# Performance work log

Measured on AMD Instinct MI355X. Metric: run time of the kernel, lower is better.

The kernel has to match this reference:

```python
import jax, jax.numpy as jnp
import numpy as np

DIM = 1024
NUM_HEADS = 16
HEAD_DIM = DIM // NUM_HEADS
ROPE_BASE = 10000.0


def _rope_tables(seq_len, head_dim, dtype):
    # inv_freq over even indices, then freqs duplicated (cat(freqs, freqs))
    inv_freq = 1.0 / (ROPE_BASE ** (jnp.arange(0, head_dim, 2, dtype=jnp.float32) / head_dim))
    t = jnp.arange(seq_len, dtype=jnp.float32)
    freqs = jnp.einsum('i,j->ij', t, inv_freq)          # [N, head_dim/2]
    emb = jnp.concatenate([freqs, freqs], axis=-1)      # [N, head_dim]
    return jnp.cos(emb).astype(dtype), jnp.sin(emb).astype(dtype)


def _rotate_half(x):
    x1, x2 = jnp.split(x, 2, axis=-1)
    return jnp.concatenate([-x2, x1], axis=-1)


def setup_inputs() -> dict:
    key = jax.random.key(0)
    k1, k2, k3 = jax.random.split(key, 3)
    B, N = 2, 2048
    x = jax.random.normal(k1, (B, N, DIM), dtype=jnp.float32)
    w_qkv = jax.random.normal(k2, (3 * DIM, DIM), dtype=jnp.float32) * (DIM ** -0.5)
    w_out = jax.random.normal(k3, (DIM, DIM), dtype=jnp.float32) * (DIM ** -0.5)
    return {"x": x, "w_qkv": w_qkv, "w_out": w_out}


def reference(x, w_qkv, w_out):
    B, N, C = x.shape
    scale = HEAD_DIM ** -0.5
    qkv = x @ w_qkv.T                                   # [B, N, 3*C]
    qkv = qkv.reshape(B, N, 3, NUM_HEADS, HEAD_DIM)
    qkv = jnp.transpose(qkv, (2, 0, 3, 1, 4))           # [3, B, H, N, hd]
    q, k, v = qkv[0], qkv[1], qkv[2]

    cos, sin = _rope_tables(N, HEAD_DIM, x.dtype)       # [N, hd] each
    q = q * cos + _rotate_half(q) * sin
    k = k * cos + _rotate_half(k) * sin

    attn = jnp.einsum('bhqd,bhkd->bhqk', q, k) * scale  # [B, H, N, N]
    attn = jax.nn.softmax(attn, axis=-1)
    out = jnp.einsum('bhqk,bhkd->bhqd', attn, v)        # [B, H, N, hd]
    out = jnp.transpose(out, (0, 2, 1, 3)).reshape(B, N, C)
    return out @ w_out.T
```

## Files before the change

### kernel.cpp

```cpp
#include <hip/hip_runtime.h>
#include <stdint.h>


#define BATCH 2
#define SEQ   2048
#define DIM_C 1024
#define NHEAD 16
#define HD    64
#define MTOT  (BATCH * SEQ)
#define NQKV  (3 * DIM_C)
#define QSCALE 0.1803368801111204f

typedef _Float16 h8 __attribute__((ext_vector_type(8)));
typedef _Float16 h4v __attribute__((ext_vector_type(4)));
typedef float    f4 __attribute__((ext_vector_type(4)));

#if __has_builtin(__builtin_amdgcn_exp2f)
#define EXP2(x) __builtin_amdgcn_exp2f(x)
#else
#define EXP2(x) exp2f(x)
#endif

__device__ __forceinline__ f4 mfma16(h8 a, h8 b, f4 c) {
  return __builtin_amdgcn_mfma_f32_16x16x32_f16(a, b, c, 0, 0, 0);
}

__device__ __forceinline__ void gload16(const _Float16* g, _Float16* l) {
  __builtin_amdgcn_global_load_lds(
      (const __attribute__((address_space(1))) void*)g,
      (__attribute__((address_space(3))) void*)l, 16, 0, 0);
}

__global__ void cvt_kernel(const float* __restrict__ src, _Float16* __restrict__ dst, int n4) {
  int stride = gridDim.x * blockDim.x;
  for (int i = blockIdx.x * blockDim.x + threadIdx.x; i < n4; i += stride) {
    float4 v = reinterpret_cast<const float4*>(src)[i];
    h4v o = {(_Float16)v.x, (_Float16)v.y, (_Float16)v.z, (_Float16)v.w};
    reinterpret_cast<h4v*>(dst)[i] = o;
  }
}

__global__ void rope_table_kernel(float* __restrict__ cosT, float* __restrict__ sinT) {
  int idx = blockIdx.x * blockDim.x + threadIdx.x;
  int n = idx >> 5, j = idx & 31;
  float inv = powf(10000.0f, -(float)(2 * j) / 64.0f);
  float a = (float)n * inv;
  cosT[idx] = cosf(a);
  sinT[idx] = sinf(a);
}

template <int OUT_F16>
__global__ __launch_bounds__(256) void gemm_nt(const _Float16* __restrict__ A,
                                               const _Float16* __restrict__ Bm,
                                               void* __restrict__ Cv,
                                               int M, int N, int K) {
  __shared__ _Float16 Ah[2][128 * 32];
  __shared__ _Float16 Bh[2][128 * 32];
  const int tid = threadIdx.x;
  const int wave = tid >> 6, lane = tid & 63;
  const int lr = lane & 15, lg = lane >> 4;
  const int m0 = blockIdx.y * 128, n0 = blockIdx.x * 128;
  const int wr = (wave >> 1) * 64, wc = (wave & 1) * 64;

  const f4 zf = {0.f, 0.f, 0.f, 0.f};
  f4 acc[4][4];
#pragma unroll
  for (int i = 0; i < 4; ++i)
#pragma unroll
    for (int j = 0; j < 4; ++j) acc[i][j] = zf;

  const _Float16* Ab = A + (size_t)m0 * K;
  const _Float16* Bb = Bm + (size_t)n0 * K;

  auto stage = [&](int ks, int bi) {
#pragma unroll
    for (int it = 0; it < 2; ++it) {
      int c = tid + it * 256;
      int row = c >> 2, part = c & 3;
      gload16(Ab + (size_t)row * K + ks * 32 + part * 8, &Ah[bi][c * 8]);
      gload16(Bb + (size_t)row * K + ks * 32 + part * 8, &Bh[bi][c * 8]);
    }
  };

  stage(0, 0);
  const int ksteps = K >> 5;
  for (int ks = 0; ks < ksteps; ++ks) {
    __syncthreads();
    int cur = ks & 1;
    if (ks + 1 < ksteps) stage(ks + 1, cur ^ 1);

    h8 af[4], bf[4];
#pragma unroll
    for (int i = 0; i < 4; ++i) af[i] = *(const h8*)&Ah[cur][(wr + i * 16 + lr) * 32 + lg * 8];
#pragma unroll
    for (int j = 0; j < 4; ++j) bf[j] = *(const h8*)&Bh[cur][(wc + j * 16 + lr) * 32 + lg * 8];
#pragma unroll
    for (int i = 0; i < 4; ++i)
#pragma unroll
      for (int j = 0; j < 4; ++j) acc[i][j] = mfma16(af[i], bf[j], acc[i][j]);
  }

#pragma unroll
  for (int i = 0; i < 4; ++i)
#pragma unroll
    for (int j = 0; j < 4; ++j)
#pragma unroll
      for (int r = 0; r < 4; ++r) {
        size_t row = (size_t)(m0 + wr + i * 16 + lg * 4 + r);
        int col = n0 + wc + j * 16 + lr;
        if (OUT_F16)
          ((_Float16*)Cv)[row * N + col] = (_Float16)acc[i][j][r];
        else
          ((float*)Cv)[row * N + col] = acc[i][j][r];
      }
}

__global__ void rope_apply_kernel(const _Float16* __restrict__ qkv,
                                  const float* __restrict__ cosT,
                                  const float* __restrict__ sinT,
                                  _Float16* __restrict__ qh,
                                  _Float16* __restrict__ kh,
                                  _Float16* __restrict__ vh) {
  int idx = blockIdx.x * blockDim.x + threadIdx.x;
  int c8 = idx & 3;
  int t = idx >> 2;
  int h = t & 15;
  t >>= 4;
  int s = t % 3;
  int m = t / 3;
  int b = m >> 11, n = m & 2047;

  const _Float16* src = qkv + (size_t)m * NQKV + s * DIM_C + h * HD + c8 * 8;
  h8 x1 = *(const h8*)src;
  h8 x2 = *(const h8*)(src + 32);
  size_t o = ((size_t)((b * NHEAD + h) * SEQ + n)) * HD + c8 * 8;

  if (s == 2) {
    *(h8*)(vh + o) = x1;
    *(h8*)(vh + o + 32) = x2;
  } else {
    f4 cs0 = *(const f4*)(cosT + n * 32 + c8 * 8);
    f4 cs1 = *(const f4*)(cosT + n * 32 + c8 * 8 + 4);
    f4 sn0 = *(const f4*)(sinT + n * 32 + c8 * 8);
    f4 sn1 = *(const f4*)(sinT + n * 32 + c8 * 8 + 4);
    float scl = (s == 0) ? QSCALE : 1.0f;
    _Float16* dst = (s == 0) ? qh : kh;
    h8 o1, o2;
#pragma unroll
    for (int j = 0; j < 8; ++j) {
      float cv = (j < 4) ? cs0[j] : cs1[j - 4];
      float sv = (j < 4) ? sn0[j] : sn1[j - 4];
      float a1 = (float)x1[j], a2 = (float)x2[j];
      o1[j] = (_Float16)((a1 * cv - a2 * sv) * scl);
      o2[j] = (_Float16)((a2 * cv + a1 * sv) * scl);
    }
    *(h8*)(dst + o) = o1;
    *(h8*)(dst + o + 32) = o2;
  }
}

__global__ void vtrans_kernel(const _Float16* __restrict__ v, _Float16* __restrict__ vt) {
  int blk = blockIdx.x;
  int bh = blk >> 6, nt = blk & 63;
  int d = threadIdx.x & 63, w = threadIdx.x >> 6;
  int n0 = nt * 32 + w * 8;
  const _Float16* src = v + (size_t)bh * SEQ * HD;
  _Float16* dst = vt + ((size_t)bh * HD + d) * SEQ;
  h8 o;
#pragma unroll
  for (int j = 0; j < 8; ++j) o[j] = src[(size_t)(n0 + j) * HD + d];
  *(h8*)(dst + n0) = o;
}

__global__ __launch_bounds__(256) void attn_kernel(const _Float16* __restrict__ qh,
                                                   const _Float16* __restrict__ kh,
                                                   const _Float16* __restrict__ vt,
                                                   _Float16* __restrict__ aoh) {
  __shared__ _Float16 Kt[2][64 * 64];
  __shared__ _Float16 Vt[2][64 * 64];
  __shared__ _Float16 PlA[4][32][40], PlB[4][32][40];

  const int tid = threadIdx.x, wave = tid >> 6, lane = tid & 63;
  const int lr = lane & 15, lg = lane >> 4;
  const int bh = blockIdx.x >> 4;
  const int qt = blockIdx.x & 15;
  const int b = bh >> 4, h = bh & 15;

  const _Float16* Qb = qh + (size_t)bh * SEQ * HD;
  const _Float16* Kb = kh + (size_t)bh * SEQ * HD;
  const _Float16* Vb = vt + (size_t)bh * HD * SEQ;
  const int q0 = qt * 128 + wave * 32;

  const int cOf0 = ((lg) ^ (lr & 7)) * 8;
  const int cOf1 = ((4 + lg) ^ (lr & 7)) * 8;

  h8 aq[2][2];
#pragma unroll
  for (int r2 = 0; r2 < 2; ++r2)
#pragma unroll
    for (int c = 0; c < 2; ++c)
      aq[r2][c] = *(const h8*)(Qb + (size_t)(q0 + r2 * 16 + lr) * HD + c * 32 + lg * 8);

  float m_s[2] = {-1e30f, -1e30f}, l_s[2] = {0.f, 0.f};
  const f4 zf = {0.f, 0.f, 0.f, 0.f};
  f4 acc[2][4];
#pragma unroll
  for (int r2 = 0; r2 < 2; ++r2)
#pragma unroll
    for (int dt = 0; dt < 4; ++dt) acc[r2][dt] = zf;

  auto stage = [&](int kt, int bi) {
    const _Float16* Ks = Kb + (size_t)kt * 64 * HD;
    const _Float16* Vs = Vb + kt * 64;
#pragma unroll
    for (int it = 0; it < 2; ++it) {
      int c = tid + it * 256;
      int row = c >> 3, part = c & 7;
      int sp = part ^ (row & 7);
      gload16(Ks + (size_t)row * HD + sp * 8, &Kt[bi][c * 8]);
      gload16(Vs + (size_t)row * SEQ + sp * 8, &Vt[bi][c * 8]);
    }
  };

  stage(0, 0);
  for (int kt = 0; kt < SEQ / 64; ++kt) {
    __syncthreads();
    const int cur = kt & 1;
    if (kt + 1 < SEQ / 64) stage(kt + 1, cur ^ 1);

    const _Float16* Kbuf = &Kt[cur][0];
    const _Float16* Vbuf = &Vt[cur][0];
    h8 bk[4][2], vb[4][2];
#pragma unroll
    for (int ct = 0; ct < 4; ++ct) {
      bk[ct][0] = *(const h8*)(Kbuf + (ct * 16 + lr) * 64 + cOf0);
      bk[ct][1] = *(const h8*)(Kbuf + (ct * 16 + lr) * 64 + cOf1);
    }
#pragma unroll
    for (int dt = 0; dt < 4; ++dt) {
      vb[dt][0] = *(const h8*)(Vbuf + (dt * 16 + lr) * 64 + cOf0);
      vb[dt][1] = *(const h8*)(Vbuf + (dt * 16 + lr) * 64 + cOf1);
    }

#pragma unroll
    for (int r2 = 0; r2 < 2; ++r2) {
      f4 St[4];
      __builtin_amdgcn_s_setprio(1);
#pragma unroll
      for (int ct = 0; ct < 4; ++ct) {
        f4 z = mfma16(bk[ct][0], aq[r2][0], zf);
        St[ct] = mfma16(bk[ct][1], aq[r2][1], z);
      }
      __builtin_amdgcn_s_setprio(0);
      float pmax = fmaxf(fmaxf(fmaxf(St[0][0], St[0][1]), fmaxf(St[0][2], St[0][3])),
                         fmaxf(fmaxf(St[1][0], St[1][1]), fmaxf(St[1][2], St[1][3])));
      float pmax2 = fmaxf(fmaxf(fmaxf(St[2][0], St[2][1]), fmaxf(St[2][2], St[2][3])),
                          fmaxf(fmaxf(St[3][0], St[3][1]), fmaxf(St[3][2], St[3][3])));
      pmax = fmaxf(pmax, pmax2);
      pmax = fmaxf(pmax, __shfl_xor(pmax, 16));
      pmax = fmaxf(pmax, __shfl_xor(pmax, 32));

      bool grow = pmax > m_s[r2] + 8.f;
      if (__ballot(grow)) {
        float mn = fmaxf(m_s[r2], pmax);
        float al = EXP2(m_s[r2] - mn);
        m_s[r2] = mn;
        l_s[r2] *= al;
#pragma unroll
        for (int dt = 0; dt < 4; ++dt)
#pragma unroll
          for (int r = 0; r < 4; ++r) acc[r2][dt][r] *= al;
      }

      float rsum = 0.f;
#pragma unroll
      for (int ct = 0; ct < 4; ++ct)
#pragma unroll
        for (int r = 0; r < 4; ++r) {
          float p = EXP2(St[ct][r] - m_s[r2]);
          St[ct][r] = p;
          rsum += p;
        }
      rsum += __shfl_xor(rsum, 16);
      rsum += __shfl_xor(rsum, 32);
      l_s[r2] += rsum;

#pragma unroll
      for (int ct = 0; ct < 4; ++ct) {
        h4v pk = {(_Float16)St[ct][0], (_Float16)St[ct][1],
                  (_Float16)St[ct][2], (_Float16)St[ct][3]};
        if (ct < 2)
          *(h4v*)&PlA[wave][r2 * 16 + lr][ct * 16 + lg * 4] = pk;
        else
          *(h4v*)&PlB[wave][r2 * 16 + lr][(ct - 2) * 16 + lg * 4] = pk;
      }
    }

    __builtin_amdgcn_s_setprio(1);
#pragma unroll
    for (int r2 = 0; r2 < 2; ++r2)
#pragma unroll
      for (int c = 0; c < 2; ++c) {
        h8 pa = (c == 0) ? *(const h8*)&PlA[wave][r2 * 16 + lr][lg * 8]
                         : *(const h8*)&PlB[wave][r2 * 16 + lr][lg * 8];
#pragma unroll
        for (int dt = 0; dt < 4; ++dt)
          acc[r2][dt] = mfma16(vb[dt][c], pa, acc[r2][dt]);
      }
    __builtin_amdgcn_s_setprio(0);
  }

#pragma unroll
  for (int r2 = 0; r2 < 2; ++r2) {
    float inv = 1.0f / l_s[r2];
    int q = q0 + r2 * 16 + lr;
#pragma unroll
    for (int dt = 0; dt < 4; ++dt) {
      h4v o = {(_Float16)(acc[r2][dt][0] * inv), (_Float16)(acc[r2][dt][1] * inv),
               (_Float16)(acc[r2][dt][2] * inv), (_Float16)(acc[r2][dt][3] * inv)};
      *(h4v*)&aoh[((size_t)(b * SEQ + q)) * DIM_C + h * HD + dt * 16 + lg * 4] = o;
    }
  }
}

extern "C" void kernel_launch(void* const* d_in, const int* in_sizes, int n_in,
                              void* d_out, int out_size, void* d_ws, size_t ws_size,
                              hipStream_t stream) {
  const float* x     = (const float*)d_in[0];
  const float* w_qkv = (const float*)d_in[1];
  const float* w_out = (const float*)d_in[2];
  float* out = (float*)d_out;

  char* w = (char*)d_ws;
  _Float16* xh    = (_Float16*)(w + 0);
  _Float16* wqkvh = (_Float16*)(w + 8388608);
  _Float16* wouth = (_Float16*)(w + 14680064);
  _Float16* qkvh  = (_Float16*)(w + 16777216);
  _Float16* qhp   = (_Float16*)(w + 41943040);
  _Float16* khp   = (_Float16*)(w + 50331648);
  _Float16* vhp   = (_Float16*)(w + 58720256);
  _Float16* aohp  = (_Float16*)(w + 67108864);
  float*    cosT  = (float*)(w + 75497472);
  float*    sinT  = (float*)(w + 75759616);
  _Float16* vtp   = (_Float16*)(w + 16777216);

  cvt_kernel<<<1024, 256, 0, stream>>>(x, xh, MTOT * DIM_C / 4);
  cvt_kernel<<<1024, 256, 0, stream>>>(w_qkv, wqkvh, NQKV * DIM_C / 4);
  cvt_kernel<<<512, 256, 0, stream>>>(w_out, wouth, DIM_C * DIM_C / 4);
  rope_table_kernel<<<SEQ * 32 / 256, 256, 0, stream>>>(cosT, sinT);

  gemm_nt<1><<<dim3(NQKV / 128, MTOT / 128), 256, 0, stream>>>(
      xh, wqkvh, (void*)qkvh, MTOT, NQKV, DIM_C);

  rope_apply_kernel<<<MTOT * 3 * NHEAD * 4 / 256, 256, 0, stream>>>(
      qkvh, cosT, sinT, qhp, khp, vhp);

  vtrans_kernel<<<32 * 64, 256, 0, stream>>>(vhp, vtp);

  attn_kernel<<<32 * (SEQ / 128), 256, 0, stream>>>(qhp, khp, vtp, aohp);

  gemm_nt<0><<<dim3(DIM_C / 128, MTOT / 128), 256, 0, stream>>>(
      aohp, wouth, (void*)out, MTOT, DIM_C, DIM_C);
}
```

Before: 156.7 us.

## Split attention KV range across two blocks and pass P through registers

The attention kernel now splits each query tile's 2048 keys into two halves handled by separate blocks. This doubles the grid from 512 to 1024 blocks to improve occupancy on the GPU's compute units, and each half writes partial outputs plus its row max and sum. A new merge kernel combines the two halves with softmax rescaling. The P matrix is also now moved into the MFMA operand layout with packed conversions and cross-lane shuffles instead of a round trip through shared memory. This removes LDS traffic, at the cost of an extra kernel launch and extra global memory traffic for the partials.

Measured after the change: 217.8 us. +39.0%, slower.

```diff
diff --git a/kernel.cpp b/kernel.cpp
--- a/kernel.cpp
+++ b/kernel.cpp
@@ -14,6 +14,7 @@
 typedef _Float16 h8 __attribute__((ext_vector_type(8)));
 typedef _Float16 h4v __attribute__((ext_vector_type(4)));
 typedef float    f4 __attribute__((ext_vector_type(4)));
+typedef unsigned int u4v __attribute__((ext_vector_type(4)));
 
 #if __has_builtin(__builtin_amdgcn_exp2f)
 #define EXP2(x) __builtin_amdgcn_exp2f(x)
@@ -23,6 +24,13 @@
 
 __device__ __forceinline__ f4 mfma16(h8 a, h8 b, f4 c) {
   return __builtin_amdgcn_mfma_f32_16x16x32_f16(a, b, c, 0, 0, 0);
+}
+
+__device__ __forceinline__ unsigned pk2(float a, float b) {
+  auto t = __builtin_amdgcn_cvt_pkrtz(a, b);
+  unsigned u;
+  __builtin_memcpy(&u, &t, 4);
+  return u;
 }
 
 __device__ __forceinline__ void gload16(const _Float16* g, _Float16* l) {
@@ -172,17 +180,20 @@
   *(h8*)(dst + n0) = o;
 }
 
-__global__ __launch_bounds__(256) void attn_kernel(const _Float16* __restrict__ qh,
-                                                   const _Float16* __restrict__ kh,
-                                                   const _Float16* __restrict__ vt,
-                                                   _Float16* __restrict__ aoh) {
+__global__ __launch_bounds__(256, 4) void attn_kernel(const _Float16* __restrict__ qh,
+                                                      const _Float16* __restrict__ kh,
+                                                      const _Float16* __restrict__ vt,
+                                                      _Float16* __restrict__ Opart,
+                                                      float* __restrict__ ml) {
   __shared__ _Float16 Kt[2][64 * 64];
   __shared__ _Float16 Vt[2][64 * 64];
-  __shared__ _Float16 PlA[4][32][40], PlB[4][32][40];
 
   const int tid = threadIdx.x, wave = tid >> 6, lane = tid & 63;
   const int lr = lane & 15, lg = lane >> 4;
-  const int bh = blockIdx.x >> 4;
+  const bool hi32 = (lane & 32) != 0;
+  const bool o16 = (lane & 16) != 0;
+  const int bh = blockIdx.x >> 5;
+  const int half = (blockIdx.x >> 4) & 1;
   const int qt = blockIdx.x & 15;
   const int b = bh >> 4, h = bh & 15;
 
@@ -190,6 +201,7 @@
   const _Float16* Kb = kh + (size_t)bh * SEQ * HD;
   const _Float16* Vb = vt + (size_t)bh * HD * SEQ;
   const int q0 = qt * 128 + wave * 32;
+  const int t0 = half * 16;
 
   const int cOf0 = ((lg) ^ (lr & 7)) * 8;
   const int cOf1 = ((4 + lg) ^ (lr & 7)) * 8;
@@ -222,11 +234,11 @@
     }
   };
 
-  stage(0, 0);
-  for (int kt = 0; kt < SEQ / 64; ++kt) {
+  stage(t0, 0);
+  for (int t = 0; t < 16; ++t) {
     __syncthreads();
-    const int cur = kt & 1;
-    if (kt + 1 < SEQ / 64) stage(kt + 1, cur ^ 1);
+    const int cur = t & 1;
+    if (t + 1 < 16) stage(t0 + t + 1, cur ^ 1);
 
     const _Float16* Kbuf = &Kt[cur][0];
     const _Float16* Vbuf = &Vt[cur][0];
@@ -285,31 +297,51 @@
       rsum += __shfl_xor(rsum, 32);
       l_s[r2] += rsum;
 
+      unsigned w[4][2];
 #pragma unroll
       for (int ct = 0; ct < 4; ++ct) {
-        h4v pk = {(_Float16)St[ct][0], (_Float16)St[ct][1],
-                  (_Float16)St[ct][2], (_Float16)St[ct][3]};
-        if (ct < 2)
-          *(h4v*)&PlA[wave][r2 * 16 + lr][ct * 16 + lg * 4] = pk;
-        else
-          *(h4v*)&PlB[wave][r2 * 16 + lr][(ct - 2) * 16 + lg * 4] = pk;
-      }
-    }
-
-    __builtin_amdgcn_s_setprio(1);
-#pragma unroll
-    for (int r2 = 0; r2 < 2; ++r2)
-#pragma unroll
-      for (int c = 0; c < 2; ++c) {
-        h8 pa = (c == 0) ? *(const h8*)&PlA[wave][r2 * 16 + lr][lg * 8]
-                         : *(const h8*)&PlB[wave][r2 * 16 + lr][lg * 8];
-#pragma unroll
-        for (int dt = 0; dt < 4; ++dt)
-          acc[r2][dt] = mfma16(vb[dt][c], pa, acc[r2][dt]);
-      }
-    __builtin_amdgcn_s_setprio(0);
-  }
-
+        w[ct][0] = pk2(St[ct][0], St[ct][1]);
+        w[ct][1] = pk2(St[ct][2], St[ct][3]);
+      }
+#pragma unroll
+      for (int s = 0; s < 2; ++s) {
+        unsigned x0 = w[0][s], y0 = w[1][s];
+        unsigned sx0 = __shfl_xor(x0, 32), sy0 = __shfl_xor(y0, 32);
+        w[0][s] = hi32 ? sy0 : x0;
+        w[1][s] = hi32 ? y0 : sx0;
+        unsigned x1 = w[2][s], y1 = w[3][s];
+        unsigned sx1 = __shfl_xor(x1, 32), sy1 = __shfl_xor(y1, 32);
+        w[2][s] = hi32 ? sy1 : x1;
+        w[3][s] = hi32 ? y1 : sx1;
+      }
+#pragma unroll
+      for (int s = 0; s < 2; ++s) {
+        unsigned x0 = w[0][s], y0 = w[1][s];
+        unsigned sx0 = __shfl_xor(x0, 16), sy0 = __shfl_xor(y0, 16);
+        w[0][s] = o16 ? sy0 : x0;
+        w[1][s] = o16 ? y0 : sx0;
+        unsigned x1 = w[2][s], y1 = w[3][s];
+        unsigned sx1 = __shfl_xor(x1, 16), sy1 = __shfl_xor(y1, 16);
+        w[2][s] = o16 ? sy1 : x1;
+        w[3][s] = o16 ? y1 : sx1;
+      }
+      u4v pw0 = {w[0][0], w[0][1], w[1][0], w[1][1]};
+      u4v pw1 = {w[2][0], w[2][1], w[3][0], w[3][1]};
+      h8 pa0, pa1;
+      __builtin_memcpy(&pa0, &pw0, 16);
+      __builtin_memcpy(&pa1, &pw1, 16);
+
+      __builtin_amdgcn_s_setprio(1);
+#pragma unroll
+      for (int dt = 0; dt < 4; ++dt) {
+        acc[r2][dt] = mfma16(vb[dt][0], pa0, acc[r2][dt]);
+        acc[r2][dt] = mfma16(vb[dt][1], pa1, acc[r2][dt]);
+      }
+      __builtin_amdgcn_s_setprio(0);
+    }
+  }
+
+  _Float16* Ob = Opart + (size_t)half * MTOT * DIM_C;
 #pragma unroll
   for (int r2 = 0; r2 < 2; ++r2) {
     float inv = 1.0f / l_s[r2];
@@ -318,9 +350,42 @@
     for (int dt = 0; dt < 4; ++dt) {
       h4v o = {(_Float16)(acc[r2][dt][0] * inv), (_Float16)(acc[r2][dt][1] * inv),
                (_Float16)(acc[r2][dt][2] * inv), (_Float16)(acc[r2][dt][3] * inv)};
-      *(h4v*)&aoh[((size_t)(b * SEQ + q)) * DIM_C + h * HD + dt * 16 + lg * 4] = o;
-    }
-  }
+      *(h4v*)&Ob[((size_t)(b * SEQ + q)) * DIM_C + h * HD + dt * 16 + lg * 4] = o;
+    }
+  }
+  if (lg == 0) {
+#pragma unroll
+    for (int r2 = 0; r2 < 2; ++r2) {
+      int q = q0 + r2 * 16 + lr;
+      *(float2*)&ml[(((size_t)half * 32 + bh) * SEQ + q) * 2] =
+          make_float2(m_s[r2], l_s[r2]);
+    }
+  }
+}
+
+__global__ void merge_kernel(const _Float16* __restrict__ Op,
+                             const float* __restrict__ ml,
+                             _Float16* __restrict__ aoh) {
+  int idx = blockIdx.x * blockDim.x + threadIdx.x;
+  int col8 = idx & 127;
+  int rq = idx >> 7;
+  int b = rq >> 11, q = rq & 2047;
+  int h = col8 >> 3;
+  int bh = b * NHEAD + h;
+  float2 ml0 = *(const float2*)&ml[((size_t)bh * SEQ + q) * 2];
+  float2 ml1 = *(const float2*)&ml[(((size_t)32 + bh) * SEQ + q) * 2];
+  float M = fmaxf(ml0.x, ml1.x);
+  float e0 = EXP2(ml0.x - M) * ml0.y;
+  float e1 = EXP2(ml1.x - M) * ml1.y;
+  float inv = 1.0f / (e0 + e1);
+  float w0 = e0 * inv, w1 = e1 * inv;
+  h8 a = ((const h8*)Op)[idx];
+  h8 c = ((const h8*)(Op + (size_t)MTOT * DIM_C))[idx];
+  h8 o;
+#pragma unroll
+  for (int j = 0; j < 8; ++j)
+    o[j] = (_Float16)(w0 * (float)a[j] + w1 * (float)c[j]);
+  ((h8*)aoh)[idx] = o;
 }
 
 extern "C" void kernel_launch(void* const* d_in, const int* in_sizes, int n_in,
@@ -333,16 +398,18 @@
 
   char* w = (char*)d_ws;
   _Float16* xh    = (_Float16*)(w + 0);
+  float*    mlp   = (float*)(w + 0);
   _Float16* wqkvh = (_Float16*)(w + 8388608);
   _Float16* wouth = (_Float16*)(w + 14680064);
   _Float16* qkvh  = (_Float16*)(w + 16777216);
+  _Float16* vtp   = (_Float16*)(w + 16777216);
+  _Float16* opart = (_Float16*)(w + 25165824);
   _Float16* qhp   = (_Float16*)(w + 41943040);
   _Float16* khp   = (_Float16*)(w + 50331648);
   _Float16* vhp   = (_Float16*)(w + 58720256);
   _Float16* aohp  = (_Float16*)(w + 67108864);
   float*    cosT  = (float*)(w + 75497472);
   float*    sinT  = (float*)(w + 75759616);
-  _Float16* vtp   = (_Float16*)(w + 16777216);
 
   cvt_kernel<<<1024, 256, 0, stream>>>(x, xh, MTOT * DIM_C / 4);
   cvt_kernel<<<1024, 256, 0, stream>>>(w_qkv, wqkvh, NQKV * DIM_C / 4);
@@ -357,7 +424,9 @@
 
   vtrans_kernel<<<32 * 64, 256, 0, stream>>>(vhp, vtp);
 
-  attn_kernel<<<32 * (SEQ / 128), 256, 0, stream>>>(qhp, khp, vtp, aohp);
+  attn_kernel<<<32 * 32, 256, 0, stream>>>(qhp, khp, vtp, opart, mlp);
+
+  merge_kernel<<<MTOT * (DIM_C / 8) / 256, 256, 0, stream>>>(opart, mlp, aohp);
 
   gemm_nt<0><<<dim3(DIM_C / 128, MTOT / 128), 256, 0, stream>>>(
       aohp, wouth, (void*)out, MTOT, DIM_C, DIM_C);
```
